# Performance work log

Hardware: AMD Instinct MI355X
Metric: run time of the kernel (lower is better)

Reference implementation:

```python
import jax, jax.numpy as jnp
import numpy as np

N, D = 16384, 128
T = 0.07


def setup_inputs() -> dict:
    key = jax.random.key(0)
    k1, k2 = jax.random.split(key)
    anchors = jax.random.normal(k1, (N, D), dtype=jnp.float32)
    positives = jax.random.normal(k2, (N, D), dtype=jnp.float32)
    return {"anchors": anchors, "positives": positives}


def reference(anchors, positives):
    # L2-normalize along feature dim (eps matches torch F.normalize default 1e-12)
    a = anchors / jnp.maximum(jnp.linalg.norm(anchors, axis=-1, keepdims=True), 1e-12)
    p = positives / jnp.maximum(jnp.linalg.norm(positives, axis=-1, keepdims=True), 1e-12)
    logits = (a @ p.T) / T  # [N, N]
    # cross-entropy with diagonal labels, mean reduction
    logz = jax.nn.logsumexp(logits, axis=-1)  # [N]
    diag = jnp.diagonal(logits)  # [N]
    return jnp.mean(logz - diag)
```

## Files before the change

kernel.cpp:

```cpp
#include <hip/hip_runtime.h>
#include <hip/hip_bf16.h>

#define N_ROWS 16384
#define DIM 128

constexpr float INV_T = 1.0f / 0.07f;
constexpr float LOG2E = 1.4426950408889634f;
constexpr float C1    = INV_T * LOG2E;
constexpr float SOP   = 4.5398160f;
constexpr float LN2   = 0.69314718055994530942f;

typedef int   v4i    __attribute__((ext_vector_type(4)));
typedef int   v8i    __attribute__((ext_vector_type(8)));
typedef float f32x16 __attribute__((ext_vector_type(16)));

typedef const __attribute__((address_space(1))) void* gptr1_t;
typedef __attribute__((address_space(3))) void*       sptr3_t;

#define TILE_BYTES 4096
#define BM 128
#define WROWS 32
#define COLSPLIT 16
#define COLS_PER (N_ROWS / COLSPLIT)
#define NJT (COLS_PER / 32)

__global__ __launch_bounds__(256) void norm_kernel(
    const float* __restrict__ A, const float* __restrict__ P,
    ushort* __restrict__ a8u, ushort* __restrict__ p8u,
    float* __restrict__ diag, float* __restrict__ sacc)
{
    if (threadIdx.x < 4) sacc[blockIdx.x * 4 + threadIdx.x] = 0.f;
    int row  = blockIdx.x * 4 + (threadIdx.x >> 6);
    int lane = threadIdx.x & 63;
    float2 av = *(const float2*)(A + (size_t)row * DIM + lane * 2);
    float2 pv = *(const float2*)(P + (size_t)row * DIM + lane * 2);
    float ssa = av.x * av.x + av.y * av.y;
    float ssp = pv.x * pv.x + pv.y * pv.y;
    float dp  = av.x * pv.x + av.y * pv.y;
    #pragma unroll
    for (int m = 1; m < 64; m <<= 1) {
        ssa += __shfl_xor(ssa, m);
        ssp += __shfl_xor(ssp, m);
        dp  += __shfl_xor(dp,  m);
    }
    float ra = 1.0f / fmaxf(sqrtf(ssa), 1e-12f);
    float rp = 1.0f / fmaxf(sqrtf(ssp), 1e-12f);
    if (lane == 0) diag[row] = dp * ra * rp * INV_T;
    float sa = ra * SOP, sp = rp * SOP;
    int apk = __builtin_amdgcn_cvt_pk_fp8_f32(av.x * sa, av.y * sa, 0, false);
    int ppk = __builtin_amdgcn_cvt_pk_fp8_f32(pv.x * sp, pv.y * sp, 0, false);
    a8u[(size_t)row * 64 + lane] = (ushort)apk;
    size_t off = (size_t)(row >> 5) * 2048 + (lane >> 5) * 1024
               + ((lane >> 4) & 1) * 512 + ((lane >> 3) & 1) * 256
               + (row & 31) * 8 + (lane & 7);
    p8u[off] = (ushort)ppk;
}

__global__ __launch_bounds__(256, 2) void lse_kernel(
    const ushort* __restrict__ a8u, const ushort* __restrict__ p8u,
    float* __restrict__ s_accum)
{
    __shared__ __attribute__((aligned(16))) char btile[3][TILE_BYTES];

    int colseg = blockIdx.x & (COLSPLIT - 1);
    int rowblk = blockIdx.x / COLSPLIT;
    int wave = threadIdx.x >> 6;
    int lane = threadIdx.x & 63;
    int c31  = lane & 31, hi = lane >> 5;
    int row0 = rowblk * BM + wave * WROWS;

    const char* a8 = (const char*)a8u;
    v8i afA0 = *(const v8i*)(a8 + (size_t)(row0 + c31) * 128 +      hi * 32);
    v8i afA1 = *(const v8i*)(a8 + (size_t)(row0 + c31) * 128 + 64 + hi * 32);

    f32x16 cinit;
    #pragma unroll
    for (int r = 0; r < 16; ++r) cinit[r] = -C1;

    float s0[16];
    #pragma unroll
    for (int r = 0; r < 16; ++r) s0[r] = 0.f;

    const char* seg = (const char*)p8u + (size_t)colseg * NJT * TILE_BYTES;
    char* lds = (char*)&btile[0][0];
    int choff = wave * 1024 + lane * 16;

    auto STAGE = [&](int t, int buf) {
        __builtin_amdgcn_global_load_lds(
            (gptr1_t)(seg + (size_t)t * TILE_BYTES + choff),
            (sptr3_t)(lds + buf * TILE_BYTES + choff), 16, 0, 0);
    };

    int rdoff = hi * 1024 + c31 * 16;

    STAGE(0, 0);
    STAGE(1, 1);

    for (int jt = 0; jt < NJT; ++jt) {
        if (jt < NJT - 1) asm volatile("s_waitcnt vmcnt(1)" ::: "memory");
        else              asm volatile("s_waitcnt vmcnt(0)" ::: "memory");
        __builtin_amdgcn_s_barrier();
        __builtin_amdgcn_sched_barrier(0);

        if (jt + 2 < NJT) STAGE(jt + 2, (jt + 2) % 3);

        const char* tb = lds + (jt % 3) * TILE_BYTES;
        v4i x0 = *(const v4i*)(tb + rdoff);
        v4i y0 = *(const v4i*)(tb + rdoff + 512);
        v4i x1 = *(const v4i*)(tb + 2048 + rdoff);
        v4i y1 = *(const v4i*)(tb + 2048 + rdoff + 512);
        v8i b0, b1;
        #pragma unroll
        for (int j = 0; j < 4; ++j) {
            b0[j] = x0[j]; b0[4 + j] = y0[j];
            b1[j] = x1[j]; b1[4 + j] = y1[j];
        }

        __builtin_amdgcn_s_setprio(1);
        f32x16 acc = __builtin_amdgcn_mfma_scale_f32_32x32x64_f8f6f4(
            afA0, b0, cinit, 0, 0, 0, 0x7f7f7f7f, 0, 0x7f7f7f7f);
        acc = __builtin_amdgcn_mfma_scale_f32_32x32x64_f8f6f4(
            afA1, b1, acc, 0, 0, 0, 0x7f7f7f7f, 0, 0x7f7f7f7f);
        __builtin_amdgcn_s_setprio(0);

        #pragma unroll
        for (int r = 0; r < 16; ++r)
            s0[r] += __builtin_amdgcn_exp2f(acc[r]);
    }

    #pragma unroll
    for (int r = 0; r < 16; ++r) {
        float v = s0[r];
        v += __shfl_xor(v, 1);
        v += __shfl_xor(v, 2);
        v += __shfl_xor(v, 4);
        v += __shfl_xor(v, 8);
        v += __shfl_xor(v, 16);
        if (c31 == 0)
            atomicAdd(&s_accum[row0 + (r & 3) + 8 * (r >> 2) + 4 * hi], v);
    }
}

__global__ __launch_bounds__(1024) void finalize_kernel(
    const float* __restrict__ s_acc, const float* __restrict__ diag,
    float* __restrict__ out)
{
    float acc = 0.f;
    int t = threadIdx.x;
    #pragma unroll
    for (int i = 0; i < 4; ++i) {
        int idx = (i * 1024 + t) * 4;
        float4 sv = *(const float4*)(s_acc + idx);
        float4 dv = *(const float4*)(diag + idx);
        acc += __builtin_amdgcn_logf(sv.x) * LN2 + INV_T - dv.x;
        acc += __builtin_amdgcn_logf(sv.y) * LN2 + INV_T - dv.y;
        acc += __builtin_amdgcn_logf(sv.z) * LN2 + INV_T - dv.z;
        acc += __builtin_amdgcn_logf(sv.w) * LN2 + INV_T - dv.w;
    }
    #pragma unroll
    for (int m = 1; m < 64; m <<= 1) acc += __shfl_xor(acc, m);
    __shared__ float wsum[16];
    if ((t & 63) == 0) wsum[t >> 6] = acc;
    __syncthreads();
    if (t == 0) {
        float r = 0.f;
        #pragma unroll
        for (int i = 0; i < 16; ++i) r += wsum[i];
        out[0] = r / (float)N_ROWS;
    }
}

extern "C" void kernel_launch(void* const* d_in, const int* in_sizes, int n_in,
                              void* d_out, int out_size, void* d_ws, size_t ws_size,
                              hipStream_t stream)
{
    const float* A = (const float*)d_in[0];
    const float* P = (const float*)d_in[1];
    float* out = (float*)d_out;

    char* ws = (char*)d_ws;
    ushort* a8u  = (ushort*)ws;
    ushort* p8u  = (ushort*)(ws + (size_t)2 * 1024 * 1024);
    float*  diag = (float*)(ws + (size_t)4 * 1024 * 1024);
    float*  sacc = (float*)(ws + (size_t)4 * 1024 * 1024 + 65536);

    norm_kernel<<<N_ROWS / 4, 256, 0, stream>>>(A, P, a8u, p8u, diag, sacc);
    lse_kernel<<<(N_ROWS / BM) * COLSPLIT, 256, 0, stream>>>(a8u, p8u, sacc);
    finalize_kernel<<<1, 1024, 0, stream>>>(sacc, diag, out);
}
```

Baseline: 61.31 us.

## Software-pipeline MFMA with exp2 accumulation using ping-pong accumulators

Restructures the column-tile loop so each iteration issues the MFMA for the next tile into a second accumulator while applying exp2 and summation to the previous tile's result. Two accumulators alternate, so the MFMA and the transcendental work can overlap instead of serializing within each iteration. The loop is unrolled by two with explicit prologue and epilogue, and it hardcodes NJT=32. This adds 16 more live accumulator registers, which may affect occupancy at 2 blocks per CU.

After: 62.41 us. No clear change (+1.8%).

```diff
diff --git a/kernel.cpp b/kernel.cpp
--- a/kernel.cpp
+++ b/kernel.cpp
@@ -93,18 +93,8 @@
 
     int rdoff = hi * 1024 + c31 * 16;
 
-    STAGE(0, 0);
-    STAGE(1, 1);
-
-    for (int jt = 0; jt < NJT; ++jt) {
-        if (jt < NJT - 1) asm volatile("s_waitcnt vmcnt(1)" ::: "memory");
-        else              asm volatile("s_waitcnt vmcnt(0)" ::: "memory");
-        __builtin_amdgcn_s_barrier();
-        __builtin_amdgcn_sched_barrier(0);
-
-        if (jt + 2 < NJT) STAGE(jt + 2, (jt + 2) % 3);
-
-        const char* tb = lds + (jt % 3) * TILE_BYTES;
+    auto MFMA_TILE = [&](int buf, f32x16& o) {
+        const char* tb = lds + buf * TILE_BYTES;
         v4i x0 = *(const v4i*)(tb + rdoff);
         v4i y0 = *(const v4i*)(tb + rdoff + 512);
         v4i x1 = *(const v4i*)(tb + 2048 + rdoff);
@@ -115,18 +105,55 @@
             b0[j] = x0[j]; b0[4 + j] = y0[j];
             b1[j] = x1[j]; b1[4 + j] = y1[j];
         }
-
         __builtin_amdgcn_s_setprio(1);
-        f32x16 acc = __builtin_amdgcn_mfma_scale_f32_32x32x64_f8f6f4(
+        o = __builtin_amdgcn_mfma_scale_f32_32x32x64_f8f6f4(
             afA0, b0, cinit, 0, 0, 0, 0x7f7f7f7f, 0, 0x7f7f7f7f);
-        acc = __builtin_amdgcn_mfma_scale_f32_32x32x64_f8f6f4(
-            afA1, b1, acc, 0, 0, 0, 0x7f7f7f7f, 0, 0x7f7f7f7f);
+        o = __builtin_amdgcn_mfma_scale_f32_32x32x64_f8f6f4(
+            afA1, b1, o, 0, 0, 0, 0x7f7f7f7f, 0, 0x7f7f7f7f);
         __builtin_amdgcn_s_setprio(0);
-
+    };
+
+    auto EXPADD = [&](const f32x16& a) {
         #pragma unroll
         for (int r = 0; r < 16; ++r)
-            s0[r] += __builtin_amdgcn_exp2f(acc[r]);
-    }
+            s0[r] += __builtin_amdgcn_exp2f(a[r]);
+    };
+
+    f32x16 accE, accO;
+
+    STAGE(0, 0);
+    STAGE(1, 1);
+
+    asm volatile("s_waitcnt vmcnt(1)" ::: "memory");
+    __builtin_amdgcn_s_barrier();
+    __builtin_amdgcn_sched_barrier(0);
+    STAGE(2, 2);
+    MFMA_TILE(0, accE);
+
+    for (int m = 0; m < 15; ++m) {
+        int jt1 = 2 * m + 1;
+        asm volatile("s_waitcnt vmcnt(1)" ::: "memory");
+        __builtin_amdgcn_s_barrier();
+        __builtin_amdgcn_sched_barrier(0);
+        STAGE(jt1 + 2, (jt1 + 2) % 3);
+        MFMA_TILE(jt1 % 3, accO);
+        EXPADD(accE);
+
+        int jt2 = 2 * m + 2;
+        asm volatile("s_waitcnt vmcnt(1)" ::: "memory");
+        __builtin_amdgcn_s_barrier();
+        __builtin_amdgcn_sched_barrier(0);
+        if (jt2 + 2 < NJT) STAGE(jt2 + 2, (jt2 + 2) % 3);
+        MFMA_TILE(jt2 % 3, accE);
+        EXPADD(accO);
+    }
+
+    asm volatile("s_waitcnt vmcnt(0)" ::: "memory");
+    __builtin_amdgcn_s_barrier();
+    __builtin_amdgcn_sched_barrier(0);
+    MFMA_TILE(31 % 3, accO);
+    EXPADD(accE);
+    EXPADD(accO);
 
     #pragma unroll
     for (int r = 0; r < 16; ++r) {
```
